# Kernel optimization log

Measured on AMD Instinct MI355X. Metric: run time of the kernel, lower is better.

## Reference

```python
import jax, jax.numpy as jnp
import numpy as np

WINDOW_SIZE = 11
SIGMA = 1.5
C3 = 1e-4
EPS = 1e-12


def _gaussian_window(channels):
    # 1D Gaussian, normalized, then outer product -> 2D separable window
    coords = jnp.arange(WINDOW_SIZE, dtype=jnp.float32) - WINDOW_SIZE // 2
    g = jnp.exp(-coords ** 2 / (2.0 * SIGMA ** 2))
    g = g / g.sum()
    w2 = g[:, None] * g[None, :]                      # [K, K]
    return jnp.broadcast_to(w2, (channels, 1, WINDOW_SIZE, WINDOW_SIZE))


def _dwconv(x, w, channels):
    # depthwise (groups=C) 2D conv with SAME-style symmetric zero padding
    pad = WINDOW_SIZE // 2
    return jax.lax.conv_general_dilated(
        x, w,
        window_strides=(1, 1),
        padding=[(pad, pad), (pad, pad)],
        dimension_numbers=('NCHW', 'OIHW', 'NCHW'),
        feature_group_count=channels,
    )


def reference(x, y):
    x = x.astype(jnp.float32)
    y = y.astype(jnp.float32)
    N, C = x.shape[0], x.shape[1]
    w = _gaussian_window(C)
    mu_x = _dwconv(x, w, C)
    mu_y = _dwconv(y, w, C)
    sigma_xy = _dwconv(x * y, w, C) - mu_x * mu_y
    sigma_x = jnp.clip(_dwconv(x * x, w, C) - mu_x * mu_x, EPS, None)
    sigma_y = jnp.clip(_dwconv(y * y, w, C) - mu_y * mu_y, EPS, None)
    structure = (sigma_xy + C3) / (jnp.sqrt(sigma_x) * jnp.sqrt(sigma_y) + C3)
    structure_mean = structure.reshape(N, C, -1).mean(axis=2)  # [N, C]
    loss = (1.0 - structure_mean).mean()
    return loss


def setup_inputs() -> dict:
    key = jax.random.key(0)
    kx, ky = jax.random.split(key)
    x = jax.random.uniform(kx, (8, 3, 512, 512), dtype=jnp.float32)
    y = jax.random.uniform(ky, (8, 3, 512, 512), dtype=jnp.float32)
    return {"x": x, "y": y}
```

## Files before the change

kernel.cpp:

```cpp
#include <hip/hip_runtime.h>

#define IMG_H 512
#define IMG_W 512
#define NPLANES 24
#define ROWS_PER_BLK 32
#define STRIPW 256
#define NITER 42
#define TOTAL_PIX 6291456.0f

__device__ __constant__ float GW[11] = {
    0.00102838f, 0.00759876f, 0.03600050f, 0.10935817f, 0.21300535f,
    0.26601172f, 0.21300535f, 0.10935817f, 0.03600050f, 0.00759876f,
    0.00102838f};

extern "C" __global__ __launch_bounds__(256) void ssim_structure_kernel(
    const float* __restrict__ x, const float* __restrict__ y,
    float* __restrict__ accum) {
  const int tid = threadIdx.x;
  const int chunk = blockIdx.x;
  const int strip = blockIdx.y;
  const int plane = blockIdx.z;

  const size_t pbase = (size_t)plane * IMG_H * IMG_W;
  const float* __restrict__ xp = x + pbase;
  const float* __restrict__ yp = y + pbase;
  const int cbase = strip * STRIPW;
  const int r0 = chunk * ROWS_PER_BLK;

  __shared__ float2 lrow[2][STRIPW + 16];

  float bx[11], by[11], bxx[11], byy[11], bxy[11];

  float acc = 0.0f;

  const int gc = cbase - 5 + tid;
  const int gc2 = gc + STRIPW;
  float2 pre_m, pre_e;

  auto loadrow = [&](int i, float2& m, float2& e) {
    const int hr = r0 - 5 + i;
    const bool rvalid = (i < NITER) & (hr >= 0) & (hr < IMG_H);
    float xv = 0.f, yv = 0.f, xe = 0.f, ye = 0.f;
    if (rvalid) {
      const int rowoff = hr * IMG_W;
      if (gc >= 0 && gc < IMG_W) {
        xv = xp[rowoff + gc];
        yv = yp[rowoff + gc];
      }
      if (tid < 10 && gc2 < IMG_W) {
        xe = xp[rowoff + gc2];
        ye = yp[rowoff + gc2];
      }
    }
    m = make_float2(xv, yv);
    e = make_float2(xe, ye);
  };

  loadrow(0, pre_m, pre_e);

  for (int ob = 0; ob < 4; ++ob) {
#pragma unroll
    for (int ii = 0; ii < 11; ++ii) {
      const int i = ob * 11 + ii;
      const int sel = i & 1;

      lrow[sel][tid] = pre_m;
      if (tid < 10) lrow[sel][STRIPW + tid] = pre_e;
      __syncthreads();

      loadrow(i + 1, pre_m, pre_e);

      if (i < NITER) {
        float tx = 0.f, ty = 0.f, txx = 0.f, tyy = 0.f, txy = 0.f;
#pragma unroll
        for (int d = 0; d < 11; ++d) {
          const float2 v = lrow[sel][tid + d];
          const float wgt = GW[d];
          const float wx = wgt * v.x;
          const float wy = wgt * v.y;
          tx += wx;
          ty += wy;
          txx = fmaf(wx, v.x, txx);
          txy = fmaf(wx, v.y, txy);
          tyy = fmaf(wy, v.y, tyy);
        }
        bx[ii] = tx;
        by[ii] = ty;
        bxx[ii] = txx;
        byy[ii] = tyy;
        bxy[ii] = txy;
      }

      if (i >= 10 && i < NITER) {
        float vx = 0.f, vy = 0.f, vxx = 0.f, vyy = 0.f, vxy = 0.f;
#pragma unroll
        for (int k = 0; k < 11; ++k) {
          const int s = (ii + 1 + k) % 11;
          const float wgt = GW[k];
          vx = fmaf(wgt, bx[s], vx);
          vy = fmaf(wgt, by[s], vy);
          vxx = fmaf(wgt, bxx[s], vxx);
          vyy = fmaf(wgt, byy[s], vyy);
          vxy = fmaf(wgt, bxy[s], vxy);
        }
        const float sxy = vxy - vx * vy;
        const float sxx = fmaxf(vxx - vx * vx, 1e-12f);
        const float syy = fmaxf(vyy - vy * vy, 1e-12f);
        const float denom = sqrtf(sxx) * sqrtf(syy) + 1e-4f;
        acc += (sxy + 1e-4f) / denom;
      }
    }
  }

#pragma unroll
  for (int off = 32; off > 0; off >>= 1) acc += __shfl_down(acc, off, 64);
  __shared__ float wsum[4];
  if ((tid & 63) == 0) wsum[tid >> 6] = acc;
  __syncthreads();
  if (tid == 0) {
    atomicAdd(accum, wsum[0] + wsum[1] + wsum[2] + wsum[3]);
  }
}

extern "C" __global__ void ssim_finalize_kernel(const float* __restrict__ accum,
                                                float* __restrict__ out) {
  out[0] = 1.0f - accum[0] * (1.0f / TOTAL_PIX);
}

extern "C" void kernel_launch(void* const* d_in, const int* in_sizes, int n_in,
                              void* d_out, int out_size, void* d_ws,
                              size_t ws_size, hipStream_t stream) {
  const float* x = (const float*)d_in[0];
  const float* y = (const float*)d_in[1];
  float* out = (float*)d_out;
  float* accum = (float*)d_ws;

  hipMemsetAsync(accum, 0, sizeof(float), stream);

  dim3 grid(IMG_H / ROWS_PER_BLK, IMG_W / STRIPW, NPLANES);
  ssim_structure_kernel<<<grid, 256, 0, stream>>>(x, y, accum);
  ssim_finalize_kernel<<<1, 1, 0, stream>>>(accum, out);
}
```

Baseline: 125.2 us.

## Restructure SSIM as vertical-first register pass with LDS horizontal pass on full rows

Each block now handles a full 512-wide row span of 8 output rows, with each thread owning two columns loaded as float2. The vertical Gaussian pass runs first, using raw pixel values held in registers. Its five moment sums go to LDS, where the horizontal pass reads them. This removes halo column loads and the strip split, which cuts per-output halo overhead. It also replaces the atomic and memset with per-block partials reduced in a parallel finalize kernel, and swaps in fast sqrt and rcp. The trade-offs are higher halo row overhead (18 rows loaded for 8 outputs), more LDS traffic and a sync per row, and approximate sqrt/rcp precision.

After: 262.3 us. 2.09x slower.

```diff
diff --git a/kernel.cpp b/kernel.cpp
--- a/kernel.cpp
+++ b/kernel.cpp
@@ -1,113 +1,132 @@
 #include <hip/hip_runtime.h>
 
-#define IMG_H 512
-#define IMG_W 512
+#define IMG 512
+#define ROWS 8
+#define NITER 18
 #define NPLANES 24
-#define ROWS_PER_BLK 32
-#define STRIPW 256
-#define NITER 42
 #define TOTAL_PIX 6291456.0f
+#define NBLOCKS (64 * 24)
 
 __device__ __constant__ float GW[11] = {
     0.00102838f, 0.00759876f, 0.03600050f, 0.10935817f, 0.21300535f,
     0.26601172f, 0.21300535f, 0.10935817f, 0.03600050f, 0.00759876f,
     0.00102838f};
 
-extern "C" __global__ __launch_bounds__(256) void ssim_structure_kernel(
+#define VSTRIDE 264
+#define QSTRIDE 528
+#define LDS_F2 2640
+
+extern "C" __global__ __launch_bounds__(256, 5) void ssim_structure_kernel(
     const float* __restrict__ x, const float* __restrict__ y,
-    float* __restrict__ accum) {
+    float* __restrict__ partial) {
   const int tid = threadIdx.x;
   const int chunk = blockIdx.x;
-  const int strip = blockIdx.y;
-  const int plane = blockIdx.z;
+  const int plane = blockIdx.y;
+  const int r0 = chunk * ROWS;
 
-  const size_t pbase = (size_t)plane * IMG_H * IMG_W;
-  const float* __restrict__ xp = x + pbase;
-  const float* __restrict__ yp = y + pbase;
-  const int cbase = strip * STRIPW;
-  const int r0 = chunk * ROWS_PER_BLK;
+  const size_t pbase = (size_t)plane * (IMG * IMG / 2);
+  const float2* __restrict__ xp = (const float2*)x + pbase;
+  const float2* __restrict__ yp = (const float2*)y + pbase;
 
-  __shared__ float2 lrow[2][STRIPW + 16];
+  __shared__ float2 vbuf[LDS_F2];
+  for (int j = tid; j < LDS_F2; j += 256) vbuf[j] = make_float2(0.f, 0.f);
+  __syncthreads();
 
-  float bx[11], by[11], bxx[11], byy[11], bxy[11];
-
+  float bx0[11], bx1[11], by0[11], by1[11];
   float acc = 0.0f;
 
-  const int gc = cbase - 5 + tid;
-  const int gc2 = gc + STRIPW;
-  float2 pre_m, pre_e;
+  float2 px, py;
+  auto loadrow = [&](int i, float2& ox, float2& oy) {
+    const int ir = r0 - 5 + i;
+    if (i < NITER && ir >= 0 && ir < IMG) {
+      const size_t off = (size_t)ir * (IMG / 2) + tid;
+      ox = xp[off];
+      oy = yp[off];
+    } else {
+      ox = make_float2(0.f, 0.f);
+      oy = make_float2(0.f, 0.f);
+    }
+  };
+  loadrow(0, px, py);
 
-  auto loadrow = [&](int i, float2& m, float2& e) {
-    const int hr = r0 - 5 + i;
-    const bool rvalid = (i < NITER) & (hr >= 0) & (hr < IMG_H);
-    float xv = 0.f, yv = 0.f, xe = 0.f, ye = 0.f;
-    if (rvalid) {
-      const int rowoff = hr * IMG_W;
-      if (gc >= 0 && gc < IMG_W) {
-        xv = xp[rowoff + gc];
-        yv = yp[rowoff + gc];
-      }
-      if (tid < 10 && gc2 < IMG_W) {
-        xe = xp[rowoff + gc2];
-        ye = yp[rowoff + gc2];
-      }
-    }
-    m = make_float2(xv, yv);
-    e = make_float2(xe, ye);
-  };
-
-  loadrow(0, pre_m, pre_e);
-
-  for (int ob = 0; ob < 4; ++ob) {
+  for (int ob = 0; ob < 2; ++ob) {
 #pragma unroll
     for (int ii = 0; ii < 11; ++ii) {
       const int i = ob * 11 + ii;
-      const int sel = i & 1;
+      if (i >= NITER) continue;
 
-      lrow[sel][tid] = pre_m;
-      if (tid < 10) lrow[sel][STRIPW + tid] = pre_e;
-      __syncthreads();
+      bx0[ii] = px.x;
+      bx1[ii] = px.y;
+      by0[ii] = py.x;
+      by1[ii] = py.y;
+      loadrow(i + 1, px, py);
 
-      loadrow(i + 1, pre_m, pre_e);
-
-      if (i < NITER) {
-        float tx = 0.f, ty = 0.f, txx = 0.f, tyy = 0.f, txy = 0.f;
-#pragma unroll
-        for (int d = 0; d < 11; ++d) {
-          const float2 v = lrow[sel][tid + d];
-          const float wgt = GW[d];
-          const float wx = wgt * v.x;
-          const float wy = wgt * v.y;
-          tx += wx;
-          ty += wy;
-          txx = fmaf(wx, v.x, txx);
-          txy = fmaf(wx, v.y, txy);
-          tyy = fmaf(wy, v.y, tyy);
-        }
-        bx[ii] = tx;
-        by[ii] = ty;
-        bxx[ii] = txx;
-        byy[ii] = tyy;
-        bxy[ii] = txy;
-      }
-
-      if (i >= 10 && i < NITER) {
-        float vx = 0.f, vy = 0.f, vxx = 0.f, vyy = 0.f, vxy = 0.f;
+      if (i >= 10) {
+        const int sel = i & 1;
+        float Vx0 = 0.f, Vx1 = 0.f, Vy0 = 0.f, Vy1 = 0.f;
+        float Vxx0 = 0.f, Vxx1 = 0.f, Vyy0 = 0.f, Vyy1 = 0.f;
+        float Vxy0 = 0.f, Vxy1 = 0.f;
 #pragma unroll
         for (int k = 0; k < 11; ++k) {
           const int s = (ii + 1 + k) % 11;
           const float wgt = GW[k];
-          vx = fmaf(wgt, bx[s], vx);
-          vy = fmaf(wgt, by[s], vy);
-          vxx = fmaf(wgt, bxx[s], vxx);
-          vyy = fmaf(wgt, byy[s], vyy);
-          vxy = fmaf(wgt, bxy[s], vxy);
+          const float wx0 = wgt * bx0[s], wx1 = wgt * bx1[s];
+          const float wy0 = wgt * by0[s], wy1 = wgt * by1[s];
+          Vx0 += wx0;
+          Vx1 += wx1;
+          Vy0 += wy0;
+          Vy1 += wy1;
+          Vxx0 = fmaf(wx0, bx0[s], Vxx0);
+          Vxx1 = fmaf(wx1, bx1[s], Vxx1);
+          Vxy0 = fmaf(wx0, by0[s], Vxy0);
+          Vxy1 = fmaf(wx1, by1[s], Vxy1);
+          Vyy0 = fmaf(wy0, by0[s], Vyy0);
+          Vyy1 = fmaf(wy1, by1[s], Vyy1);
         }
-        const float sxy = vxy - vx * vy;
-        const float sxx = fmaxf(vxx - vx * vx, 1e-12f);
-        const float syy = fmaxf(vyy - vy * vy, 1e-12f);
-        const float denom = sqrtf(sxx) * sqrtf(syy) + 1e-4f;
-        acc += (sxy + 1e-4f) / denom;
+        const int wbase = sel * VSTRIDE + 3 + tid;
+        vbuf[0 * QSTRIDE + wbase] = make_float2(Vx0, Vx1);
+        vbuf[1 * QSTRIDE + wbase] = make_float2(Vy0, Vy1);
+        vbuf[2 * QSTRIDE + wbase] = make_float2(Vxx0, Vxx1);
+        vbuf[3 * QSTRIDE + wbase] = make_float2(Vyy0, Vyy1);
+        vbuf[4 * QSTRIDE + wbase] = make_float2(Vxy0, Vxy1);
+        __syncthreads();
+
+        float S0[5], S1[5];
+#pragma unroll
+        for (int q = 0; q < 5; ++q) {
+          const float2* arr = vbuf + q * QSTRIDE + sel * VSTRIDE + tid;
+          float a[14];
+#pragma unroll
+          for (int d = 0; d < 7; ++d) {
+            const float2 v = arr[d];
+            a[2 * d] = v.x;
+            a[2 * d + 1] = v.y;
+          }
+          float s0 = 0.f, s1 = 0.f;
+#pragma unroll
+          for (int d = 0; d < 11; ++d) {
+            s0 = fmaf(GW[d], a[d + 1], s0);
+            s1 = fmaf(GW[d], a[d + 2], s1);
+          }
+          S0[q] = s0;
+          S1[q] = s1;
+        }
+        {
+          const float mx = S0[0], my = S0[1];
+          const float sxy = fmaf(-mx, my, S0[4]);
+          const float sxx = fmaxf(fmaf(-mx, mx, S0[2]), 1e-12f);
+          const float syy = fmaxf(fmaf(-my, my, S0[3]), 1e-12f);
+          const float den = __builtin_amdgcn_sqrtf(sxx * syy) + 1e-4f;
+          acc += (sxy + 1e-4f) * __builtin_amdgcn_rcpf(den);
+        }
+        {
+          const float mx = S1[0], my = S1[1];
+          const float sxy = fmaf(-mx, my, S1[4]);
+          const float sxx = fmaxf(fmaf(-mx, mx, S1[2]), 1e-12f);
+          const float syy = fmaxf(fmaf(-my, my, S1[3]), 1e-12f);
+          const float den = __builtin_amdgcn_sqrtf(sxx * syy) + 1e-4f;
+          acc += (sxy + 1e-4f) * __builtin_amdgcn_rcpf(den);
+        }
       }
     }
   }
@@ -118,13 +137,23 @@
   if ((tid & 63) == 0) wsum[tid >> 6] = acc;
   __syncthreads();
   if (tid == 0) {
-    atomicAdd(accum, wsum[0] + wsum[1] + wsum[2] + wsum[3]);
+    partial[blockIdx.y * 64 + blockIdx.x] = wsum[0] + wsum[1] + wsum[2] + wsum[3];
   }
 }
 
-extern "C" __global__ void ssim_finalize_kernel(const float* __restrict__ accum,
+extern "C" __global__ void ssim_finalize_kernel(const float* __restrict__ partial,
                                                 float* __restrict__ out) {
-  out[0] = 1.0f - accum[0] * (1.0f / TOTAL_PIX);
+  const int tid = threadIdx.x;
+  float s = 0.f;
+  for (int j = tid; j < NBLOCKS; j += 256) s += partial[j];
+#pragma unroll
+  for (int off = 32; off > 0; off >>= 1) s += __shfl_down(s, off, 64);
+  __shared__ float wsum[4];
+  if ((tid & 63) == 0) wsum[tid >> 6] = s;
+  __syncthreads();
+  if (tid == 0) {
+    out[0] = 1.0f - (wsum[0] + wsum[1] + wsum[2] + wsum[3]) * (1.0f / TOTAL_PIX);
+  }
 }
 
 extern "C" void kernel_launch(void* const* d_in, const int* in_sizes, int n_in,
@@ -133,11 +162,9 @@
   const float* x = (const float*)d_in[0];
   const float* y = (const float*)d_in[1];
   float* out = (float*)d_out;
-  float* accum = (float*)d_ws;
+  float* partial = (float*)d_ws;
 
-  hipMemsetAsync(accum, 0, sizeof(float), stream);
-
-  dim3 grid(IMG_H / ROWS_PER_BLK, IMG_W / STRIPW, NPLANES);
-  ssim_structure_kernel<<<grid, 256, 0, stream>>>(x, y, accum);
-  ssim_finalize_kernel<<<1, 1, 0, stream>>>(accum, out);
+  dim3 grid(IMG / ROWS, NPLANES, 1);
+  ssim_structure_kernel<<<grid, 256, 0, stream>>>(x, y, partial);
+  ssim_finalize_kernel<<<1, 256, 0, stream>>>(partial, out);
 }
```
